# Kernel tuning notes

Measured on AMD Instinct MI355X. Metric: run time of the kernel, lower is better.

The kernel has to match this reference:

```python
import jax, jax.numpy as jnp
import numpy as np

D_MODEL = 2048
N_QUERY = 4
N_HEAD = 8
D_HEAD = D_MODEL // (N_QUERY * N_HEAD)  # 64
D_KV = D_HEAD * N_HEAD                  # 512
BATCH, SEQ = 2, 2048


def setup_inputs() -> dict:
    key = jax.random.key(0)
    ks = jax.random.split(key, 5)
    w_scale = 1.0 / np.sqrt(D_MODEL).astype(np.float32)
    x = jax.random.normal(ks[0], (BATCH, SEQ, D_MODEL), jnp.float32)
    Wq = jax.random.normal(ks[1], (D_MODEL, D_MODEL), jnp.float32) * w_scale
    Wk = jax.random.normal(ks[2], (D_KV, D_MODEL), jnp.float32) * w_scale
    Wv = jax.random.normal(ks[3], (D_KV, D_MODEL), jnp.float32) * w_scale
    memory = jax.random.normal(ks[4], (D_KV, D_KV), jnp.float32) * 0.02
    memory_norm = jnp.ones((D_KV, 1), jnp.float32)
    memory_weight = jnp.ones((1,), jnp.float32)
    return dict(x=x, Wq=Wq, Wk=Wk, Wv=Wv, memory=memory,
                memory_norm=memory_norm, memory_weight=memory_weight)


def reference(x, Wq, Wk, Wv, memory, memory_norm, memory_weight):
    b, s, d = x.shape
    # projections (torch Linear: y = x @ W.T, no bias)
    q = x @ Wq.T                              # [b, s, d_model]
    k = x @ Wk.T                              # [b, s, d_kv]
    v = x @ Wv.T                              # [b, s, d_kv]

    # --- A_dot: grouped (shared-KV) scaled dot-product attention ---
    qh = q.reshape(b, s, N_QUERY, N_HEAD, D_HEAD)
    kh = k.reshape(b, s, N_HEAD, D_HEAD)
    vh = v.reshape(b, s, N_HEAD, D_HEAD)
    scale = np.float32(1.0 / np.sqrt(np.float32(D_HEAD)))
    scores = jnp.einsum('bsqhd,bthd->bqhst', qh, kh) * scale  # [b,nq,nh,s,s]
    probs = jax.nn.softmax(scores, axis=-1)
    a_dot = jnp.einsum('bqhst,bthd->bsqhd', probs, vh)
    a_dot = a_dot.reshape(b, s, N_QUERY * N_HEAD, D_HEAD)

    # --- A_mem: linear-attention memory read (Infini-attention Eq. 7) ---
    sigma_q = jax.nn.elu(q.reshape(b, s, N_QUERY, D_KV))        # [b,s,nq,d_kv]
    a_mem = (sigma_q @ memory) / (sigma_q @ memory_norm)        # [b,s,nq,d_kv]
    a_mem = a_mem.reshape(b, s, N_QUERY * N_HEAD, D_HEAD)

    # --- fuse with learned scalar gate (Eq. 10) ---
    w = jax.nn.sigmoid(memory_weight)  # shape (1,), broadcasts like torch scalar
    out = a_dot * (1.0 - w) + a_mem * w
    return out.reshape(b, s, D_MODEL)
```

## Files before the change

### kernel.cpp

```cpp
#include <hip/hip_runtime.h>
#include <hip/hip_bf16.h>
#include <math.h>

#define D_MODEL 2048
#define N_QUERY 4
#define N_HEAD  8
#define D_HEAD  64
#define D_KV    512
#define BATCH   2
#define SEQ     2048
#define BS      (BATCH*SEQ)
#define MROWS   (BS*N_QUERY)
#define NQKV    3072

typedef __attribute__((ext_vector_type(8)))  short bf16x8;
typedef __attribute__((ext_vector_type(4)))  float f32x4;
typedef __attribute__((ext_vector_type(16))) float f32x16;
typedef unsigned short u16;
typedef unsigned int   u32;

union Frag { bf16x8 v; u32 w[4]; };

__device__ __forceinline__ f32x4 mfma16(bf16x8 a, bf16x8 b, f32x4 c) {
    return __builtin_amdgcn_mfma_f32_16x16x32_bf16(a, b, c, 0, 0, 0);
}
__device__ __forceinline__ f32x16 mfma32(bf16x8 a, bf16x8 b, f32x16 c) {
    return __builtin_amdgcn_mfma_f32_32x32x16_bf16(a, b, c, 0, 0, 0);
}
__device__ __forceinline__ u16 f32_to_bf16(float f) {
    u32 u = __float_as_uint(f);
    u32 r = (u + 0x7fffu + ((u >> 16) & 1u)) >> 16;
    return (u16)r;
}
__device__ __forceinline__ float bf16_to_f32(u16 h) {
    return __uint_as_float(((u32)h) << 16);
}
__device__ __forceinline__ u32 cvt_pk_bf16(float lo, float hi) {
    u32 r;
    asm volatile("v_cvt_pk_bf16_f32 %0, %1, %2" : "=v"(r) : "v"(lo), "v"(hi));
    return r;
}
__device__ __forceinline__ float exp2_fast(float x) {
#if __has_builtin(__builtin_amdgcn_exp2f)
    return __builtin_amdgcn_exp2f(x);
#else
    return exp2f(x);
#endif
}
__device__ __forceinline__ void load_lds16(const void* g, void* l) {
    using GP = const __attribute__((address_space(1))) unsigned char*;
    using LP = __attribute__((address_space(3))) unsigned char*;
    __builtin_amdgcn_global_load_lds(
        reinterpret_cast<GP>(reinterpret_cast<uintptr_t>(g)),
        reinterpret_cast<LP>(reinterpret_cast<uintptr_t>(l)), 16, 0, 0);
}

__global__ __launch_bounds__(256) void prep(const float* __restrict__ x,   u16* __restrict__ xb,
                                            const float* __restrict__ Wq,  u16* __restrict__ wq,
                                            const float* __restrict__ Wk,  u16* __restrict__ wk,
                                            const float* __restrict__ Wv,  u16* __restrict__ wv,
                                            const float* __restrict__ mem, u16* __restrict__ mtb) {
    const int bx = blockIdx.x;
    if (bx >= 2048) {
        __shared__ float tile[32][33];
        const int j  = bx - 2048;
        const int c0 = (j & 15) * 32, r0 = (j >> 4) * 32;
        const int tr = threadIdx.x >> 3, tc = (threadIdx.x & 7) * 4;
        float4 v = *(const float4*)(mem + (size_t)(r0 + tr) * D_KV + c0 + tc);
        tile[tr][tc+0]=v.x; tile[tr][tc+1]=v.y; tile[tr][tc+2]=v.z; tile[tr][tc+3]=v.w;
        __syncthreads();
        ushort4 o;
        o.x = f32_to_bf16(tile[tc+0][tr]);
        o.y = f32_to_bf16(tile[tc+1][tr]);
        o.z = f32_to_bf16(tile[tc+2][tr]);
        o.w = f32_to_bf16(tile[tc+3][tr]);
        *(ushort4*)(mtb + (size_t)(c0 + tr) * D_KV + r0 + tc) = o;
        return;
    }
    const float* in; u16* out; int n4, blk, nblk;
    if (bx < 1024)      { in = x;  out = xb; n4 = BS*D_MODEL/4;      blk = bx;        nblk = 1024; }
    else if (bx < 1536) { in = Wq; out = wq; n4 = D_MODEL*D_MODEL/4; blk = bx - 1024; nblk = 512;  }
    else if (bx < 1792) { in = Wk; out = wk; n4 = D_KV*D_MODEL/4;    blk = bx - 1536; nblk = 256;  }
    else                { in = Wv; out = wv; n4 = D_KV*D_MODEL/4;    blk = bx - 1792; nblk = 256;  }
    for (int i = blk*256 + threadIdx.x; i < n4; i += nblk*256) {
        float4 v = ((const float4*)in)[i];
        ushort4 o;
        o.x = f32_to_bf16(v.x); o.y = f32_to_bf16(v.y);
        o.z = f32_to_bf16(v.z); o.w = f32_to_bf16(v.w);
        ((ushort4*)out)[i] = o;
    }
}

__global__ __launch_bounds__(256) void gemm_qkv(const u16* __restrict__ A,
                                                const u16* __restrict__ Wf,
                                                u16* __restrict__ Cq,
                                                u16* __restrict__ Ck,
                                                u16* __restrict__ Vt) {
    __shared__ __align__(16) u16 As[128*32];
    __shared__ __align__(16) u16 Bs[128*32];
    const int K = D_MODEL;
    const int tid  = threadIdx.x;
    const int lane = tid & 63;
    const int wid  = tid >> 6;
    const int m0 = blockIdx.y * 128, n0 = blockIdx.x * 128;
    const int wr = (wid >> 1) * 64, wc = (wid & 1) * 64;
    const int lq = lane & 15, lg = lane >> 4;
    const int srow = tid >> 2;
    const int scol = (tid & 3) * 8;
    f32x4 acc[4][4] = {};
    const u16* Ag = A  + (size_t)(m0 + srow) * K + scol;
    const u16* Wg = Wf + (size_t)(n0 + srow) * K + scol;
    for (int k0 = 0; k0 < K; k0 += 32) {
        __syncthreads();
        load_lds16(Ag + k0,                 &As[srow*32 + scol]);
        load_lds16(Ag + k0 + (size_t)64*K,  &As[(srow+64)*32 + scol]);
        load_lds16(Wg + k0,                 &Bs[srow*32 + scol]);
        load_lds16(Wg + k0 + (size_t)64*K,  &Bs[(srow+64)*32 + scol]);
        __syncthreads();
        bf16x8 a[4], b[4];
        #pragma unroll
        for (int mi = 0; mi < 4; ++mi)
            a[mi] = *(const bf16x8*)&As[(wr + mi*16 + lq)*32 + lg*8];
        #pragma unroll
        for (int ni = 0; ni < 4; ++ni)
            b[ni] = *(const bf16x8*)&Bs[(wc + ni*16 + lq)*32 + lg*8];
        #pragma unroll
        for (int mi = 0; mi < 4; ++mi)
            #pragma unroll
            for (int ni = 0; ni < 4; ++ni)
                acc[mi][ni] = mfma16(a[mi], b[ni], acc[mi][ni]);
    }
    if (n0 < D_MODEL) {
        #pragma unroll
        for (int mi = 0; mi < 4; ++mi)
            #pragma unroll
            for (int ni = 0; ni < 4; ++ni)
                #pragma unroll
                for (int r = 0; r < 4; ++r)
                    Cq[(size_t)(m0 + wr + mi*16 + lg*4 + r) * D_MODEL + n0 + wc + ni*16 + lq] =
                        f32_to_bf16(acc[mi][ni][r]);
    } else if (n0 < D_MODEL + D_KV) {
        const int col = n0 - D_MODEL;
        #pragma unroll
        for (int mi = 0; mi < 4; ++mi)
            #pragma unroll
            for (int ni = 0; ni < 4; ++ni)
                #pragma unroll
                for (int r = 0; r < 4; ++r)
                    Ck[(size_t)(m0 + wr + mi*16 + lg*4 + r) * D_KV + col + wc + ni*16 + lq] =
                        f32_to_bf16(acc[mi][ni][r]);
    } else {
        const int cbase = n0 - (D_MODEL + D_KV);
        #pragma unroll
        for (int mi = 0; mi < 4; ++mi) {
            int row = m0 + wr + mi*16 + lg*4;
            int bb  = row >> 11;
            int seq = row & (SEQ - 1);
            #pragma unroll
            for (int ni = 0; ni < 4; ++ni) {
                int col = cbase + wc + ni*16 + lq;
                union { u16 h[4]; uint2 d; } t;
                #pragma unroll
                for (int r = 0; r < 4; ++r) t.h[r] = f32_to_bf16(acc[mi][ni][r]);
                *(uint2*)(Vt + ((size_t)(bb * D_KV + col)) * SEQ + seq) = t.d;
            }
        }
    }
}

#define PACK_P(sc0, sc1, pf)  do {                                          \
    u32 Wp[8][2];                                                           \
    _Pragma("unroll")                                                       \
    for (int q = 0; q < 4; ++q) {                                           \
        Wp[q][0]   = cvt_pk_bf16(sc0[4*q],   sc0[4*q+1]);                   \
        Wp[q][1]   = cvt_pk_bf16(sc0[4*q+2], sc0[4*q+3]);                   \
        Wp[4+q][0] = cvt_pk_bf16(sc1[4*q],   sc1[4*q+1]);                   \
        Wp[4+q][1] = cvt_pk_bf16(sc1[4*q+2], sc1[4*q+3]);                   \
    }                                                                       \
    _Pragma("unroll")                                                       \
    for (int s = 0; s < 4; ++s) {                                           \
        const int b0 = (s >> 1)*4 + 2*(s & 1);                              \
        u32 a0 = Wp[b0][0], c0 = Wp[b0+1][0];                               \
        u32 a1 = Wp[b0][1], c1 = Wp[b0+1][1];                               \
        asm("v_permlane32_swap_b32 %0, %1" : "+v"(a0), "+v"(c0));           \
        asm("v_permlane32_swap_b32 %0, %1" : "+v"(a1), "+v"(c1));           \
        pf[s].w[0] = a0; pf[s].w[1] = a1;                                   \
        pf[s].w[2] = c0; pf[s].w[3] = c1;                                   \
    }                                                                       \
} while (0)

__global__ __launch_bounds__(256, 2) void attn_mfma(const u16* __restrict__ qb,
                                                    const u16* __restrict__ kb,
                                                    const u16* __restrict__ vtb,
                                                    float* __restrict__ out,
                                                    const float* __restrict__ mw) {
    __shared__ __align__(16) u16 Ks [2][4096];
    __shared__ __align__(16) u16 VTs[2][4096];
    const int tid = threadIdx.x, lane = tid & 63, wid = tid >> 6;
    const int lq = lane & 31, hl = lane >> 5;
    const int swz   = (blockIdx.x & 7) * 64 + (blockIdx.x >> 3);
    const int qtile = swz & 31;
    const int bh    = swz >> 5;
    const int b = bh >> 3, h = bh & 7;
    const int s0 = qtile * 64;
    const int qcol = wid * D_KV + h * D_HEAD;
    const size_t rowbase = (size_t)b * SEQ;

    bf16x8 qA[4], qB[4];
    {
        const float C = 0.18033688011112042f;
        const u16* qsA = qb + (rowbase + s0 + lq)      * D_MODEL + qcol + 8*hl;
        const u16* qsB = qb + (rowbase + s0 + 32 + lq) * D_MODEL + qcol + 8*hl;
        #pragma unroll
        for (int s = 0; s < 4; ++s) {
            bf16x8 ta = *(const bf16x8*)(qsA + 16*s);
            bf16x8 tb = *(const bf16x8*)(qsB + 16*s);
            #pragma unroll
            for (int e = 0; e < 8; ++e) {
                ta[e] = (short)f32_to_bf16(bf16_to_f32((u16)ta[e]) * C);
                tb[e] = (short)f32_to_bf16(bf16_to_f32((u16)tb[e]) * C);
            }
            qA[s] = ta; qB[s] = tb;
        }
    }

    const char* kbase = (const char*)(kb + rowbase * D_KV + h * D_HEAD);
    const char* vbase = (const char*)(vtb + ((size_t)b * D_KV + h * D_HEAD) * SEQ);
    int ksrc_off[2], vsrc_off[2];
    #pragma unroll
    for (int c = 0; c < 2; ++c) {
        int o   = c*4096 + tid*16;
        int row = o >> 7;
        int col = (o & 127) ^ ((row & 7) << 4);
        ksrc_off[c] = row*(D_KV*2) + col;
        vsrc_off[c] = row*(SEQ*2) + col;
    }

    f32x16 o0A = {}, o1A = {}, o0B = {}, o1B = {};
    float lsA = 0.f, lsB = 0.f;

    const int NT = SEQ / 64;
    #pragma unroll
    for (int c = 0; c < 2; ++c) {
        load_lds16(kbase + ksrc_off[c], (char*)Ks[0]  + c*4096 + tid*16);
        load_lds16(vbase + vsrc_off[c], (char*)VTs[0] + c*4096 + tid*16);
    }

    const int swl = (lq & 7) << 4;
    for (int j = 0; j < NT; ++j) {
        const int buf = j & 1;
        __syncthreads();
        if (j + 1 < NT) {
            const char* kj = kbase + (size_t)(j+1)*64*(D_KV*2);
            const char* vj = vbase + (size_t)(j+1)*128;
            #pragma unroll
            for (int c = 0; c < 2; ++c) {
                load_lds16(kj + ksrc_off[c], (char*)Ks[buf^1]  + c*4096 + tid*16);
                load_lds16(vj + vsrc_off[c], (char*)VTs[buf^1] + c*4096 + tid*16);
            }
        }

        f32x16 sA0 = {}, sA1 = {}, sB0 = {}, sB1 = {};
        const char* Kc = (const char*)Ks[buf];
        __builtin_amdgcn_s_setprio(1);
        #pragma unroll
        for (int s = 0; s < 4; ++s) {
            int col = 32*s + 16*hl;
            bf16x8 k0 = *(const bf16x8*)(Kc + (( lq      *128 + col) ^ swl));
            bf16x8 k1 = *(const bf16x8*)(Kc + (((lq + 32)*128 + col) ^ swl));
            sA0 = mfma32(k0, qA[s], sA0);
            sB0 = mfma32(k0, qB[s], sB0);
            sA1 = mfma32(k1, qA[s], sA1);
            sB1 = mfma32(k1, qB[s], sB1);
        }
        __builtin_amdgcn_s_setprio(0);

        float tA = 0.f, tB = 0.f;
        #pragma unroll
        for (int i = 0; i < 16; ++i) { sA0[i] = exp2_fast(sA0[i]); tA += sA0[i]; }
        #pragma unroll
        for (int i = 0; i < 16; ++i) { sA1[i] = exp2_fast(sA1[i]); tA += sA1[i]; }
        #pragma unroll
        for (int i = 0; i < 16; ++i) { sB0[i] = exp2_fast(sB0[i]); tB += sB0[i]; }
        #pragma unroll
        for (int i = 0; i < 16; ++i) { sB1[i] = exp2_fast(sB1[i]); tB += sB1[i]; }
        lsA += tA; lsB += tB;

        Frag pfA[4], pfB[4];
        PACK_P(sA0, sA1, pfA);
        PACK_P(sB0, sB1, pfB);

        const char* Vc = (const char*)VTs[buf];
        __builtin_amdgcn_s_setprio(1);
        #pragma unroll
        for (int s = 0; s < 4; ++s) {
            int col = 32*s + 16*hl;
            bf16x8 v0 = *(const bf16x8*)(Vc + (( lq      *128 + col) ^ swl));
            bf16x8 v1 = *(const bf16x8*)(Vc + (((lq + 32)*128 + col) ^ swl));
            o0A = mfma32(v0, pfA[s].v, o0A);
            o0B = mfma32(v0, pfB[s].v, o0B);
            o1A = mfma32(v1, pfA[s].v, o1A);
            o1B = mfma32(v1, pfB[s].v, o1B);
        }
        __builtin_amdgcn_s_setprio(0);
    }

    float lA = lsA + __shfl_xor(lsA, 32);
    float lB = lsB + __shfl_xor(lsB, 32);
    const float w = 1.f / (1.f + __expf(-mw[0]));
    const float invA = (1.f - w) / lA;
    const float invB = (1.f - w) / lB;
    float* dstA = out + (rowbase + s0 + lq)      * D_MODEL + qcol;
    float* dstB = out + (rowbase + s0 + 32 + lq) * D_MODEL + qcol;
    #pragma unroll
    for (int g = 0; g < 4; ++g) {
        int dbase = 8*g + 4*hl;
        *(float4*)(dstA + dbase) =
            make_float4(o0A[4*g]*invA, o0A[4*g+1]*invA, o0A[4*g+2]*invA, o0A[4*g+3]*invA);
        *(float4*)(dstA + 32 + dbase) =
            make_float4(o1A[4*g]*invA, o1A[4*g+1]*invA, o1A[4*g+2]*invA, o1A[4*g+3]*invA);
        *(float4*)(dstB + dbase) =
            make_float4(o0B[4*g]*invB, o0B[4*g+1]*invB, o0B[4*g+2]*invB, o0B[4*g+3]*invB);
        *(float4*)(dstB + 32 + dbase) =
            make_float4(o1B[4*g]*invB, o1B[4*g+1]*invB, o1B[4*g+2]*invB, o1B[4*g+3]*invB);
    }
}

__global__ __launch_bounds__(256) void mem_gemm_mfma(const u16* __restrict__ qbuf,
                                                     const u16* __restrict__ MT,
                                                     const float* __restrict__ mn,
                                                     float* __restrict__ out,
                                                     const float* __restrict__ mw) {
    __shared__ __align__(16) u16 As[128*32];
    __shared__ __align__(16) u16 Bs[128*32];
    __shared__ float den_s[128];
    const int tid  = threadIdx.x;
    const int lane = tid & 63;
    const int wid  = tid >> 6;
    const int i0 = blockIdx.y * 128, n0 = blockIdx.x * 128;
    const int wr = (wid >> 1) * 64, wc = (wid & 1) * 64;
    const int lq = lane & 15, lg = lane >> 4;
    const int srow = tid >> 2;
    const int scol = (tid & 3) * 8;
    f32x4 acc[4][4] = {};
    float dpart0 = 0.f, dpart1 = 0.f;
    const u16* Bg = MT + (size_t)(n0 + srow) * D_KV + scol;
    for (int k0 = 0; k0 < D_KV; k0 += 32) {
        __syncthreads();
        float4 mn0 = *(const float4*)(mn + k0 + scol);
        float4 mn1 = *(const float4*)(mn + k0 + scol + 4);
        float mnr[8] = {mn0.x, mn0.y, mn0.z, mn0.w, mn1.x, mn1.y, mn1.z, mn1.w};
        #pragma unroll
        for (int half = 0; half < 2; ++half) {
            int row = half*64 + srow;
            bf16x8 v = *(const bf16x8*)(qbuf + (size_t)(i0 + row) * D_KV + k0 + scol);
            bf16x8 ov;
            float dp = 0.f;
            #pragma unroll
            for (int e = 0; e < 8; ++e) {
                float xv = bf16_to_f32((u16)v[e]);
                float el = xv > 0.f ? xv : __expf(xv) - 1.f;
                dp += el * mnr[e];
                ov[e] = (short)f32_to_bf16(el);
            }
            if (half) dpart1 += dp; else dpart0 += dp;
            *(bf16x8*)&As[row*32 + scol] = ov;
        }
        load_lds16(Bg + k0,                     &Bs[srow*32 + scol]);
        load_lds16(Bg + k0 + (size_t)64*D_KV,   &Bs[(srow+64)*32 + scol]);
        __syncthreads();
        bf16x8 a[4], b[4];
        #pragma unroll
        for (int mi = 0; mi < 4; ++mi)
            a[mi] = *(const bf16x8*)&As[(wr + mi*16 + lq)*32 + lg*8];
        #pragma unroll
        for (int ni = 0; ni < 4; ++ni)
            b[ni] = *(const bf16x8*)&Bs[(wc + ni*16 + lq)*32 + lg*8];
        #pragma unroll
        for (int mi = 0; mi < 4; ++mi)
            #pragma unroll
            for (int ni = 0; ni < 4; ++ni)
                acc[mi][ni] = mfma16(a[mi], b[ni], acc[mi][ni]);
    }
    dpart0 += __shfl_xor(dpart0, 1);  dpart0 += __shfl_xor(dpart0, 2);
    dpart1 += __shfl_xor(dpart1, 1);  dpart1 += __shfl_xor(dpart1, 2);
    if ((tid & 3) == 0) { den_s[srow] = dpart0; den_s[srow + 64] = dpart1; }
    __syncthreads();
    const float w = 1.f / (1.f + __expf(-mw[0]));
    #pragma unroll
    for (int mi = 0; mi < 4; ++mi)
        #pragma unroll
        for (int r = 0; r < 4; ++r) {
            int rl  = wr + mi*16 + lg*4 + r;
            float g = w / den_s[rl];
            int row = i0 + rl;
            #pragma unroll
            for (int ni = 0; ni < 4; ++ni) {
                float* dst = out + (size_t)row * D_KV + n0 + wc + ni*16 + lq;
                *dst += acc[mi][ni][r] * g;
            }
        }
}

extern "C" void kernel_launch(void* const* d_in, const int* in_sizes, int n_in,
                              void* d_out, int out_size, void* d_ws, size_t ws_size,
                              hipStream_t stream) {
    const float* x   = (const float*)d_in[0];
    const float* Wq  = (const float*)d_in[1];
    const float* Wk  = (const float*)d_in[2];
    const float* Wv  = (const float*)d_in[3];
    const float* mem = (const float*)d_in[4];
    const float* mn  = (const float*)d_in[5];
    const float* mw  = (const float*)d_in[6];
    float* out = (float*)d_out;

    u16* qb  = (u16*)d_ws;
    u16* kb  = qb  + (size_t)BS * D_MODEL;
    u16* xb  = kb  + (size_t)BS * D_KV;
    u16* vtb = xb  + (size_t)BS * D_MODEL;
    u16* mtb = vtb + (size_t)BATCH * D_KV * SEQ;
    u16* wf  = (u16*)d_out;

    prep<<<2304, 256, 0, stream>>>(x, xb,
                                   Wq, wf,
                                   Wk, wf + (size_t)D_MODEL*D_MODEL,
                                   Wv, wf + (size_t)(D_MODEL+D_KV)*D_MODEL,
                                   mem, mtb);
    gemm_qkv<<<dim3(NQKV/128, BS/128), 256, 0, stream>>>(xb, wf, qb, kb, vtb);
    attn_mfma<<<dim3(SEQ/64 * BATCH*N_HEAD), 256, 0, stream>>>(qb, kb, vtb, out, mw);
    mem_gemm_mfma<<<dim3(D_KV/128, MROWS/128), 256, 0, stream>>>(qb, mtb, mn, out, mw);
}
```

Baseline: 185.8 us.

## Double-buffer QKV GEMM LDS tiles with XOR swizzle and block remap

The QKV projection GEMM now prefetches the next K-slice into a second LDS buffer while computing the current one, which drops one barrier per iteration. The LDS layout gets an XOR swizzle to cut bank conflicts on fragment reads. The grid is flattened to 1D and remapped so that consecutive blocks go to different XCDs while tiles that share A rows stay grouped, aiming for better L2 reuse. LDS use doubles, which may lower occupancy.

```diff
diff --git a/kernel.cpp b/kernel.cpp
--- a/kernel.cpp
+++ b/kernel.cpp
@@ -96,39 +96,65 @@
                                                 u16* __restrict__ Cq,
                                                 u16* __restrict__ Ck,
                                                 u16* __restrict__ Vt) {
-    __shared__ __align__(16) u16 As[128*32];
-    __shared__ __align__(16) u16 Bs[128*32];
+    __shared__ __align__(16) u16 As[2][128*32];
+    __shared__ __align__(16) u16 Bs[2][128*32];
     const int K = D_MODEL;
     const int tid  = threadIdx.x;
     const int lane = tid & 63;
     const int wid  = tid >> 6;
-    const int m0 = blockIdx.y * 128, n0 = blockIdx.x * 128;
+    const int swzb = (blockIdx.x & 7) * 96 + (blockIdx.x >> 3);
+    const int mt = swzb / 24, nt = swzb - mt * 24;
+    const int m0 = mt * 128, n0 = nt * 128;
     const int wr = (wid >> 1) * 64, wc = (wid & 1) * 64;
     const int lq = lane & 15, lg = lane >> 4;
-    const int srow = tid >> 2;
-    const int scol = (tid & 3) * 8;
     f32x4 acc[4][4] = {};
-    const u16* Ag = A  + (size_t)(m0 + srow) * K + scol;
-    const u16* Wg = Wf + (size_t)(n0 + srow) * K + scol;
+    int soff[2];
+    #pragma unroll
+    for (int c = 0; c < 2; ++c) {
+        int o   = c*4096 + tid*16;
+        int row = o >> 6;
+        int cb  = (o & 63) ^ ((row & 3) << 4);
+        soff[c] = row * (K*2) + cb;
+    }
+    const char* Ag = (const char*)(A  + (size_t)m0 * K);
+    const char* Wg = (const char*)(Wf + (size_t)n0 * K);
+    #pragma unroll
+    for (int c = 0; c < 2; ++c) {
+        load_lds16(Ag + soff[c], (char*)As[0] + c*4096 + tid*16);
+        load_lds16(Wg + soff[c], (char*)Bs[0] + c*4096 + tid*16);
+    }
+    __syncthreads();
+    int cur = 0;
     for (int k0 = 0; k0 < K; k0 += 32) {
-        __syncthreads();
-        load_lds16(Ag + k0,                 &As[srow*32 + scol]);
-        load_lds16(Ag + k0 + (size_t)64*K,  &As[(srow+64)*32 + scol]);
-        load_lds16(Wg + k0,                 &Bs[srow*32 + scol]);
-        load_lds16(Wg + k0 + (size_t)64*K,  &Bs[(srow+64)*32 + scol]);
-        __syncthreads();
+        if (k0 + 32 < K) {
+            #pragma unroll
+            for (int c = 0; c < 2; ++c) {
+                load_lds16(Ag + (size_t)(k0 + 32)*2 + soff[c],
+                           (char*)As[cur^1] + c*4096 + tid*16);
+                load_lds16(Wg + (size_t)(k0 + 32)*2 + soff[c],
+                           (char*)Bs[cur^1] + c*4096 + tid*16);
+            }
+        }
         bf16x8 a[4], b[4];
-        #pragma unroll
-        for (int mi = 0; mi < 4; ++mi)
-            a[mi] = *(const bf16x8*)&As[(wr + mi*16 + lq)*32 + lg*8];
-        #pragma unroll
-        for (int ni = 0; ni < 4; ++ni)
-            b[ni] = *(const bf16x8*)&Bs[(wc + ni*16 + lq)*32 + lg*8];
+        const char* Ac = (const char*)As[cur];
+        const char* Bc = (const char*)Bs[cur];
+        #pragma unroll
+        for (int mi = 0; mi < 4; ++mi) {
+            int row = wr + mi*16 + lq;
+            a[mi] = *(const bf16x8*)(Ac + ((row*64 + lg*16) ^ ((row & 3) << 4)));
+        }
+        #pragma unroll
+        for (int ni = 0; ni < 4; ++ni) {
+            int row = wc + ni*16 + lq;
+            b[ni] = *(const bf16x8*)(Bc + ((row*64 + lg*16) ^ ((row & 3) << 4)));
+        }
         #pragma unroll
         for (int mi = 0; mi < 4; ++mi)
             #pragma unroll
             for (int ni = 0; ni < 4; ++ni)
                 acc[mi][ni] = mfma16(a[mi], b[ni], acc[mi][ni]);
+        __syncthreads();
+        cur ^= 1;
     }
     if (n0 < D_MODEL) {
         #pragma unroll
@@ -426,7 +452,7 @@
                                    Wk, wf + (size_t)D_MODEL*D_MODEL,
                                    Wv, wf + (size_t)(D_MODEL+D_KV)*D_MODEL,
                                    mem, mtb);
-    gemm_qkv<<<dim3(NQKV/128, BS/128), 256, 0, stream>>>(xb, wf, qb, kb, vtb);
+    gemm_qkv<<<768, 256, 0, stream>>>(xb, wf, qb, kb, vtb);
     attn_mfma<<<dim3(SEQ/64 * BATCH*N_HEAD), 256, 0, stream>>>(qb, kb, vtb, out, mw);
     mem_gemm_mfma<<<dim3(D_KV/128, MROWS/128), 256, 0, stream>>>(qb, mtb, mn, out, mw);
 }
```

Result: no change. 187.0 us (+0.6%).
